# Kernel tuning notes

Hardware: AMD Instinct MI355X
Metric: run time of the kernel (lower is better)

Reference implementation:

```python
import jax, jax.numpy as jnp
import numpy as np

B, Q, S, T, H = 8, 64, 64, 64, 768
NH, HD = 12, 64  # head_num, head_dim


def setup_inputs() -> dict:
    key = jax.random.key(0)
    k1, k2, k3, k4, k5, k6, k7 = jax.random.split(key, 7)
    ini_q = jax.random.normal(k1, (B, Q, H), dtype=jnp.float32)
    ini_k = jax.random.normal(k2, (B, S, T, H), dtype=jnp.float32)
    mask = jax.random.randint(k3, (B, S, T), 0, 2).astype(jnp.float32)  # 1 = masked
    # learned params (Linear weights stored as [in, out] for x @ W)
    sc = 1.0 / np.sqrt(H)
    Wq = jax.random.normal(k4, (H, H), dtype=jnp.float32) * sc
    Wkv = jax.random.normal(k5, (H, H), dtype=jnp.float32) * sc
    Wo = jax.random.normal(k6, (H, H), dtype=jnp.float32) * sc
    bo = jax.random.normal(k7, (H,), dtype=jnp.float32) * 0.02
    return {"ini_q": ini_q, "ini_k": ini_k, "mask": mask,
            "Wq": Wq, "Wkv": Wkv, "Wo": Wo, "bo": bo}


def reference(ini_q, ini_k, mask, Wq, Wkv, Wo, bo):
    batch, q_num, _ = ini_q.shape
    _, s_num, t_num, _ = ini_k.shape
    scale = 1.0 / np.sqrt(HD)
    q = (ini_q @ Wq).reshape(batch, q_num, NH, HD)
    kv = (ini_k @ Wkv).reshape(batch, s_num, t_num, NH, HD)  # k == v
    # [b, h, q, s, t]
    scores = jnp.einsum('bqhd,bsthd->bhqst', q, kv) * scale
    scores = scores + mask[:, None, None, :, :] * -10000.0
    alpha = jax.nn.softmax(scores, axis=4)  # dropout is identity in eval
    res = jnp.einsum('bhqst,bsthd->bqshd', alpha, kv).reshape(batch, q_num, s_num, NH * HD)
    return res @ Wo + bo
```

## Files before the change

kernel.cpp:

```cpp
#include <hip/hip_runtime.h>
#include <stdint.h>


typedef __bf16 bf16_t;
typedef __attribute__((ext_vector_type(8))) __bf16 bf16x8;
typedef __attribute__((ext_vector_type(4))) __bf16 bf16x4;
typedef __attribute__((ext_vector_type(4))) float f32x4;

#define HDIM 768

__device__ __forceinline__ void gload16(const bf16_t* g, bf16_t* l) {
  __builtin_amdgcn_global_load_lds(
      (const __attribute__((address_space(1))) void*)g,
      (__attribute__((address_space(3))) void*)l, 16, 0, 0);
}

__global__ __launch_bounds__(256) void splitT_kernel(const float* __restrict__ w,
                                                     bf16_t* __restrict__ hT,
                                                     bf16_t* __restrict__ lT) {
  int idx = blockIdx.x * 256 + threadIdx.x;
  int k = idx / HDIM, n = idx % HDIM;
  float v = w[idx];
  bf16_t hb = (bf16_t)v;
  hT[n * HDIM + k] = hb;
  lT[n * HDIM + k] = (bf16_t)(v - (float)hb);
}

template <int EPI, bool AF32>
__global__ __launch_bounds__(256) void gemm_kernel(
    const float* __restrict__ Agf,
    const bf16_t* __restrict__ Agh, const bf16_t* __restrict__ Agl,
    const bf16_t* __restrict__ Bgh, const bf16_t* __restrict__ Bgl,
    bf16_t* __restrict__ Ch, bf16_t* __restrict__ Cl,
    bf16_t* __restrict__ CTh, bf16_t* __restrict__ CTl,
    float* __restrict__ Cf, const float* __restrict__ bias) {
  __shared__ bf16_t sAh[128 * 32], sAl[128 * 32], sBh[128 * 32], sBl[128 * 32];
  const int nwg = gridDim.x;
  const int cpx = nwg >> 3;
  const int g = blockIdx.x;
  const int wg = (g & 7) * cpx + (g >> 3);
  const int bn = wg % 6, bm = wg / 6;
  const int tid = threadIdx.x, lane = tid & 63, w = tid >> 6;
  const int wr = (w >> 1) * 64, wc = (w & 1) * 64;
  const int l15 = lane & 15, l4 = lane >> 4;
  f32x4 acc[4][4] = {};

  for (int kt = 0; kt < 24; ++kt) {
    const int k0 = kt * 32;
    __syncthreads();
    if constexpr (AF32) {
#pragma unroll
      for (int j = 0; j < 4; ++j) {
        const int c = tid + j * 256;
        const int row = c >> 3, cg = c & 7;
        const float4 v4 =
            *(const float4*)&Agf[(size_t)(bm * 128 + row) * HDIM + k0 + cg * 4];
        const float vv[4] = {v4.x, v4.y, v4.z, v4.w};
        bf16x4 hv, lv;
#pragma unroll
        for (int e = 0; e < 4; ++e) {
          bf16_t hb = (bf16_t)vv[e];
          hv[e] = hb;
          lv[e] = (bf16_t)(vv[e] - (float)hb);
        }
        *(bf16x4*)&sAh[row * 32 + cg * 4] = hv;
        *(bf16x4*)&sAl[row * 32 + cg * 4] = lv;
      }
    } else {
#pragma unroll
      for (int j = 0; j < 2; ++j) {
        const int c0 = j * 256 + w * 64;
        const int c = c0 + lane;
        const int row = c >> 2, cg = c & 3;
        const size_t ga = (size_t)(bm * 128 + row) * HDIM + k0 + cg * 8;
        gload16(&Agh[ga], &sAh[c0 * 8]);
        gload16(&Agl[ga], &sAl[c0 * 8]);
      }
    }
#pragma unroll
    for (int j = 0; j < 2; ++j) {
      const int c0 = j * 256 + w * 64;
      const int c = c0 + lane;
      const int row = c >> 2, cg = c & 3;
      const size_t gb = (size_t)(bn * 128 + row) * HDIM + k0 + cg * 8;
      gload16(&Bgh[gb], &sBh[c0 * 8]);
      gload16(&Bgl[gb], &sBl[c0 * 8]);
    }
    __syncthreads();
    bf16x8 a_h[4], a_l[4], b_h[4], b_l[4];
#pragma unroll
    for (int m = 0; m < 4; ++m) {
      const int ra = (wr + m * 16 + l15) * 32 + l4 * 8;
      a_h[m] = *(const bf16x8*)&sAh[ra];
      a_l[m] = *(const bf16x8*)&sAl[ra];
      const int rb = (wc + m * 16 + l15) * 32 + l4 * 8;
      b_h[m] = *(const bf16x8*)&sBh[rb];
      b_l[m] = *(const bf16x8*)&sBl[rb];
    }
#pragma unroll
    for (int m = 0; m < 4; ++m)
#pragma unroll
      for (int n = 0; n < 4; ++n) {
        acc[m][n] = __builtin_amdgcn_mfma_f32_16x16x32_bf16(a_h[m], b_h[n], acc[m][n], 0, 0, 0);
        acc[m][n] = __builtin_amdgcn_mfma_f32_16x16x32_bf16(a_h[m], b_l[n], acc[m][n], 0, 0, 0);
        acc[m][n] = __builtin_amdgcn_mfma_f32_16x16x32_bf16(a_l[m], b_h[n], acc[m][n], 0, 0, 0);
      }
  }
#pragma unroll
  for (int m = 0; m < 4; ++m)
#pragma unroll
    for (int n = 0; n < 4; ++n) {
      const int row0 = bm * 128 + wr + m * 16 + l4 * 4;
      const int col = bn * 128 + wc + n * 16 + l15;
      if constexpr (EPI == 1) {
        const float bv = bias[col];
#pragma unroll
        for (int j = 0; j < 4; ++j)
          Cf[(size_t)(row0 + j) * HDIM + col] = acc[m][n][j] + bv;
      } else if constexpr (EPI == 0) {
#pragma unroll
        for (int j = 0; j < 4; ++j) {
          const float v = acc[m][n][j];
          const bf16_t hb = (bf16_t)v;
          Ch[(size_t)(row0 + j) * HDIM + col] = hb;
          Cl[(size_t)(row0 + j) * HDIM + col] = (bf16_t)(v - (float)hb);
        }
      } else {
        bf16x4 hv, lv;
#pragma unroll
        for (int j = 0; j < 4; ++j) {
          const float v = acc[m][n][j];
          const bf16_t hb = (bf16_t)v;
          hv[j] = hb;
          lv[j] = (bf16_t)(v - (float)hb);
        }
        const int b = row0 >> 12, s = (row0 >> 6) & 63, t0 = row0 & 63;
        const int hh = col >> 6, d = col & 63;
        const size_t tb =
            ((size_t)((b * 64 + s) * 12 + hh)) * 4096 + d * 64 + t0;
        *(bf16x4*)&CTh[tb] = hv;
        *(bf16x4*)&CTl[tb] = lv;
      }
    }
}

__global__ __launch_bounds__(256) void attn_kernel(
    const bf16_t* __restrict__ qh, const bf16_t* __restrict__ ql,
    const bf16_t* __restrict__ kvTh, const bf16_t* __restrict__ kvTl,
    const float* __restrict__ mask,
    bf16_t* __restrict__ resh, bf16_t* __restrict__ resl) {
  const int s = blockIdx.x, hh = blockIdx.y, b = blockIdx.z;
  const int tid = threadIdx.x, lane = tid & 63, w = tid >> 6;
  const int l15 = lane & 15, l4 = lane >> 4;
  const int LDT = 72, LDP = 68;
  __shared__ __align__(16) char smemA[64 * 72 * 2 * 2];
  __shared__ __align__(16) bf16_t Ph[64 * 72], Pl[64 * 72];
  __shared__ float mk[64];
  bf16_t* Kh = (bf16_t*)smemA;
  bf16_t* Kl = Kh + 64 * 72;
  float* OldsF = (float*)smemA;

  if (tid < 64) mk[tid] = mask[((size_t)b * 64 + s) * 64 + tid] * -10000.0f;

  const size_t tb0 = ((size_t)((b * 64 + s) * 12 + hh)) * 4096;
#pragma unroll
  for (int j = 0; j < 2; ++j) {
    const int cg = j * 4 + w;
    const bf16x8 vh = *(const bf16x8*)&kvTh[tb0 + (size_t)lane * 64 + cg * 8];
    const bf16x8 vl = *(const bf16x8*)&kvTl[tb0 + (size_t)lane * 64 + cg * 8];
#pragma unroll
    for (int e = 0; e < 8; ++e) {
      Kh[(cg * 8 + e) * LDT + lane] = vh[e];
      Kl[(cg * 8 + e) * LDT + lane] = vl[e];
    }
  }

  const size_t qbase = ((size_t)(b * 64 + w * 16 + l15)) * HDIM + hh * 64;
  bf16x8 qh8[2], ql8[2];
#pragma unroll
  for (int ks = 0; ks < 2; ++ks) {
    qh8[ks] = *(const bf16x8*)&qh[qbase + ks * 32 + l4 * 8];
    ql8[ks] = *(const bf16x8*)&ql[qbase + ks * 32 + l4 * 8];
  }
  __syncthreads();

  f32x4 St[4] = {};
#pragma unroll
  for (int ks = 0; ks < 2; ++ks) {
#pragma unroll
    for (int mf = 0; mf < 4; ++mf) {
      const int ra = (mf * 16 + l15) * LDT + ks * 32 + l4 * 8;
      const bf16x8 kh8 = *(const bf16x8*)&Kh[ra];
      const bf16x8 kl8 = *(const bf16x8*)&Kl[ra];
      St[mf] = __builtin_amdgcn_mfma_f32_16x16x32_bf16(kh8, qh8[ks], St[mf], 0, 0, 0);
      St[mf] = __builtin_amdgcn_mfma_f32_16x16x32_bf16(kh8, ql8[ks], St[mf], 0, 0, 0);
      St[mf] = __builtin_amdgcn_mfma_f32_16x16x32_bf16(kl8, qh8[ks], St[mf], 0, 0, 0);
    }
  }

  float p[16];
  float mx = -1e30f;
#pragma unroll
  for (int mf = 0; mf < 4; ++mf)
#pragma unroll
    for (int j = 0; j < 4; ++j) {
      const float v = St[mf][j] * 0.125f + mk[mf * 16 + l4 * 4 + j];
      p[mf * 4 + j] = v;
      mx = fmaxf(mx, v);
    }
  mx = fmaxf(mx, __shfl_xor(mx, 16));
  mx = fmaxf(mx, __shfl_xor(mx, 32));
  float sum = 0.f;
#pragma unroll
  for (int i = 0; i < 16; ++i) {
    const float e = __expf(p[i] - mx);
    p[i] = e;
    sum += e;
  }
  sum += __shfl_xor(sum, 16);
  sum += __shfl_xor(sum, 32);
  const float inv = 1.0f / sum;

  const int q = w * 16 + l15;
#pragma unroll
  for (int mf = 0; mf < 4; ++mf) {
    bf16x4 hv, lv;
#pragma unroll
    for (int j = 0; j < 4; ++j) {
      const float v = p[mf * 4 + j] * inv;
      const bf16_t hb = (bf16_t)v;
      hv[j] = hb;
      lv[j] = (bf16_t)(v - (float)hb);
    }
    *(bf16x4*)&Ph[q * LDT + mf * 16 + l4 * 4] = hv;
    *(bf16x4*)&Pl[q * LDT + mf * 16 + l4 * 4] = lv;
  }
  __syncthreads();

  f32x4 Ot[4] = {};
  const size_t ab = tb0 + (size_t)(w * 16 + l15) * 64;
#pragma unroll
  for (int ks = 0; ks < 2; ++ks) {
    const bf16x8 ah = *(const bf16x8*)&kvTh[ab + ks * 32 + l4 * 8];
    const bf16x8 al = *(const bf16x8*)&kvTl[ab + ks * 32 + l4 * 8];
#pragma unroll
    for (int nf = 0; nf < 4; ++nf) {
      const int rb = (nf * 16 + l15) * LDT + ks * 32 + l4 * 8;
      const bf16x8 ph8 = *(const bf16x8*)&Ph[rb];
      const bf16x8 pl8 = *(const bf16x8*)&Pl[rb];
      Ot[nf] = __builtin_amdgcn_mfma_f32_16x16x32_bf16(ah, ph8, Ot[nf], 0, 0, 0);
      Ot[nf] = __builtin_amdgcn_mfma_f32_16x16x32_bf16(ah, pl8, Ot[nf], 0, 0, 0);
      Ot[nf] = __builtin_amdgcn_mfma_f32_16x16x32_bf16(al, ph8, Ot[nf], 0, 0, 0);
    }
  }
#pragma unroll
  for (int nf = 0; nf < 4; ++nf)
    *(f32x4*)&OldsF[(nf * 16 + l15) * LDP + w * 16 + l4 * 4] = Ot[nf];
  __syncthreads();

  const int qq = tid >> 2, ch = tid & 3;
  float vv[16];
#pragma unroll
  for (int k = 0; k < 4; ++k) {
    const f32x4 t4 = *(const f32x4*)&OldsF[qq * LDP + ch * 16 + k * 4];
    vv[k * 4 + 0] = t4[0]; vv[k * 4 + 1] = t4[1];
    vv[k * 4 + 2] = t4[2]; vv[k * 4 + 3] = t4[3];
  }
  bf16x8 h8[2], l8[2];
#pragma unroll
  for (int k = 0; k < 16; ++k) {
    const float v = vv[k];
    const bf16_t hb = (bf16_t)v;
    h8[k >> 3][k & 7] = hb;
    l8[k >> 3][k & 7] = (bf16_t)(v - (float)hb);
  }
  const size_t rb = ((size_t)((b * 64 + qq) * 64 + s)) * HDIM + hh * 64 + ch * 16;
  *(bf16x8*)&resh[rb] = h8[0];
  *(bf16x8*)&resh[rb + 8] = h8[1];
  *(bf16x8*)&resl[rb] = l8[0];
  *(bf16x8*)&resl[rb + 8] = l8[1];
}

extern "C" void kernel_launch(void* const* d_in, const int* in_sizes, int n_in,
                              void* d_out, int out_size, void* d_ws, size_t ws_size,
                              hipStream_t stream) {
  const float* ini_q = (const float*)d_in[0];
  const float* ini_k = (const float*)d_in[1];
  const float* mask = (const float*)d_in[2];
  const float* Wq = (const float*)d_in[3];
  const float* Wkv = (const float*)d_in[4];
  const float* Wo = (const float*)d_in[5];
  const float* bo = (const float*)d_in[6];
  float* out = (float*)d_out;

  const size_t SQ = 512ull * HDIM;
  const size_t SK = 32768ull * HDIM;
  const size_t SW = 768ull * HDIM;

  char* p = (char*)d_ws;
  auto carve = [&](size_t bytes) {
    char* r = p;
    p += (bytes + 255) & ~(size_t)255;
    return r;
  };
  bf16_t* wq_h = (bf16_t*)carve(SW * 2);
  bf16_t* wq_l = (bf16_t*)carve(SW * 2);
  bf16_t* wkv_h = (bf16_t*)carve(SW * 2);
  bf16_t* wkv_l = (bf16_t*)carve(SW * 2);
  bf16_t* wo_h = (bf16_t*)carve(SW * 2);
  bf16_t* wo_l = (bf16_t*)carve(SW * 2);
  bf16_t* q_h = (bf16_t*)carve(SQ * 2);
  bf16_t* q_l = (bf16_t*)carve(SQ * 2);
  bf16_t* kvT_h = (bf16_t*)carve(SK * 2);
  bf16_t* kvT_l = (bf16_t*)carve(SK * 2);
  bf16_t* res_h = (bf16_t*)carve(SK * 2);
  bf16_t* res_l = (bf16_t*)carve(SK * 2);
  if ((size_t)(p - (char*)d_ws) > ws_size) return;

  splitT_kernel<<<dim3(SW / 256), 256, 0, stream>>>(Wq, wq_h, wq_l);
  splitT_kernel<<<dim3(SW / 256), 256, 0, stream>>>(Wkv, wkv_h, wkv_l);
  splitT_kernel<<<dim3(SW / 256), 256, 0, stream>>>(Wo, wo_h, wo_l);

  gemm_kernel<0, true><<<dim3(24), 256, 0, stream>>>(
      ini_q, nullptr, nullptr, wq_h, wq_l, q_h, q_l, nullptr, nullptr,
      nullptr, nullptr);
  gemm_kernel<2, true><<<dim3(1536), 256, 0, stream>>>(
      ini_k, nullptr, nullptr, wkv_h, wkv_l, nullptr, nullptr, kvT_h, kvT_l,
      nullptr, nullptr);
  attn_kernel<<<dim3(64, 12, 8), 256, 0, stream>>>(q_h, q_l, kvT_h, kvT_l,
                                                   mask, res_h, res_l);
  gemm_kernel<1, false><<<dim3(1536), 256, 0, stream>>>(
      nullptr, res_h, res_l, wo_h, wo_l, nullptr, nullptr, nullptr, nullptr,
      out, bo);
}
```

Baseline: 541.9 us.

## Restructure attention to loop over s with double-buffered K and dual KV layouts

The KV projection GEMM now writes both a transposed and a natural-layout copy of the split bf16 KV. The attention kernel processes 8 s-slices per block, double-buffering the natural-layout K tile into XOR-swizzled LDS via async global-to-LDS loads, and reads V directly from global in transposed layout. It also writes results directly instead of transposing through LDS. GEMM LDS tiles get XOR swizzling or padding to reduce bank conflicts. The cost is extra global writes for the second KV copy and scattered 2-byte result stores.

```diff
diff --git a/kernel.cpp b/kernel.cpp
--- a/kernel.cpp
+++ b/kernel.cpp
@@ -33,8 +33,11 @@
     const bf16_t* __restrict__ Bgh, const bf16_t* __restrict__ Bgl,
     bf16_t* __restrict__ Ch, bf16_t* __restrict__ Cl,
     bf16_t* __restrict__ CTh, bf16_t* __restrict__ CTl,
+    bf16_t* __restrict__ CNh, bf16_t* __restrict__ CNl,
     float* __restrict__ Cf, const float* __restrict__ bias) {
-  __shared__ bf16_t sAh[128 * 32], sAl[128 * 32], sBh[128 * 32], sBl[128 * 32];
+  const int LDA = AF32 ? 40 : 32;
+  __shared__ bf16_t sAh[128 * 40], sAl[128 * 40];
+  __shared__ bf16_t sBh[128 * 32], sBl[128 * 32];
   const int nwg = gridDim.x;
   const int cpx = nwg >> 3;
   const int g = blockIdx.x;
@@ -63,16 +66,17 @@
           hv[e] = hb;
           lv[e] = (bf16_t)(vv[e] - (float)hb);
         }
-        *(bf16x4*)&sAh[row * 32 + cg * 4] = hv;
-        *(bf16x4*)&sAl[row * 32 + cg * 4] = lv;
+        *(bf16x4*)&sAh[row * 40 + cg * 4] = hv;
+        *(bf16x4*)&sAl[row * 40 + cg * 4] = lv;
       }
     } else {
 #pragma unroll
       for (int j = 0; j < 2; ++j) {
         const int c0 = j * 256 + w * 64;
         const int c = c0 + lane;
-        const int row = c >> 2, cg = c & 3;
-        const size_t ga = (size_t)(bm * 128 + row) * HDIM + k0 + cg * 8;
+        const int row = c >> 2, slot = c & 3;
+        const size_t ga = (size_t)(bm * 128 + row) * HDIM + k0 +
+                          ((slot ^ ((row >> 1) & 3)) * 8);
         gload16(&Agh[ga], &sAh[c0 * 8]);
         gload16(&Agl[ga], &sAl[c0 * 8]);
       }
@@ -81,8 +85,9 @@
     for (int j = 0; j < 2; ++j) {
       const int c0 = j * 256 + w * 64;
       const int c = c0 + lane;
-      const int row = c >> 2, cg = c & 3;
-      const size_t gb = (size_t)(bn * 128 + row) * HDIM + k0 + cg * 8;
+      const int row = c >> 2, slot = c & 3;
+      const size_t gb = (size_t)(bn * 128 + row) * HDIM + k0 +
+                        ((slot ^ ((row >> 1) & 3)) * 8);
       gload16(&Bgh[gb], &sBh[c0 * 8]);
       gload16(&Bgl[gb], &sBl[c0 * 8]);
     }
@@ -90,10 +95,13 @@
     bf16x8 a_h[4], a_l[4], b_h[4], b_l[4];
 #pragma unroll
     for (int m = 0; m < 4; ++m) {
-      const int ra = (wr + m * 16 + l15) * 32 + l4 * 8;
+      const int rowa = wr + m * 16 + l15;
+      const int ra = AF32 ? rowa * 40 + l4 * 8
+                          : rowa * 32 + ((l4 ^ ((rowa >> 1) & 3)) * 8);
       a_h[m] = *(const bf16x8*)&sAh[ra];
       a_l[m] = *(const bf16x8*)&sAl[ra];
-      const int rb = (wc + m * 16 + l15) * 32 + l4 * 8;
+      const int rowb = wc + m * 16 + l15;
+      const int rb = rowb * 32 + ((l4 ^ ((rowb >> 1) & 3)) * 8);
       b_h[m] = *(const bf16x8*)&sBh[rb];
       b_l[m] = *(const bf16x8*)&sBl[rb];
     }
@@ -136,149 +144,159 @@
         }
         const int b = row0 >> 12, s = (row0 >> 6) & 63, t0 = row0 & 63;
         const int hh = col >> 6, d = col & 63;
-        const size_t tb =
-            ((size_t)((b * 64 + s) * 12 + hh)) * 4096 + d * 64 + t0;
-        *(bf16x4*)&CTh[tb] = hv;
-        *(bf16x4*)&CTl[tb] = lv;
-      }
-    }
-}
-
-__global__ __launch_bounds__(256) void attn_kernel(
+        const size_t base = ((size_t)((b * 64 + s) * 12 + hh)) * 4096;
+        *(bf16x4*)&CTh[base + d * 64 + t0] = hv;
+        *(bf16x4*)&CTl[base + d * 64 + t0] = lv;
+#pragma unroll
+        for (int j = 0; j < 4; ++j) {
+          CNh[base + (t0 + j) * 64 + d] = hv[j];
+          CNl[base + (t0 + j) * 64 + d] = lv[j];
+        }
+      }
+    }
+}
+
+__device__ __forceinline__ void stage_k(const bf16_t* __restrict__ gh,
+                                        const bf16_t* __restrict__ gl,
+                                        bf16_t* lh, bf16_t* ll,
+                                        int w, int lane) {
+#pragma unroll
+  for (int j = 0; j < 2; ++j) {
+    const int c0 = j * 256 + w * 64;
+    const int c = c0 + lane;
+    const int t = c >> 3, sl = c & 7;
+    const int srcd = (sl ^ (t & 7)) * 8;
+    gload16(&gh[t * 64 + srcd], &lh[c0 * 8]);
+    gload16(&gl[t * 64 + srcd], &ll[c0 * 8]);
+  }
+}
+
+__global__ __launch_bounds__(256, 3) void attn_kernel(
     const bf16_t* __restrict__ qh, const bf16_t* __restrict__ ql,
+    const bf16_t* __restrict__ kvNh, const bf16_t* __restrict__ kvNl,
     const bf16_t* __restrict__ kvTh, const bf16_t* __restrict__ kvTl,
     const float* __restrict__ mask,
     bf16_t* __restrict__ resh, bf16_t* __restrict__ resl) {
-  const int s = blockIdx.x, hh = blockIdx.y, b = blockIdx.z;
+  const int sq = blockIdx.x, hh = blockIdx.y, b = blockIdx.z;
+  const int s0 = sq * 8;
   const int tid = threadIdx.x, lane = tid & 63, w = tid >> 6;
   const int l15 = lane & 15, l4 = lane >> 4;
-  const int LDT = 72, LDP = 68;
-  __shared__ __align__(16) char smemA[64 * 72 * 2 * 2];
-  __shared__ __align__(16) bf16_t Ph[64 * 72], Pl[64 * 72];
-  __shared__ float mk[64];
-  bf16_t* Kh = (bf16_t*)smemA;
-  bf16_t* Kl = Kh + 64 * 72;
-  float* OldsF = (float*)smemA;
-
-  if (tid < 64) mk[tid] = mask[((size_t)b * 64 + s) * 64 + tid] * -10000.0f;
-
-  const size_t tb0 = ((size_t)((b * 64 + s) * 12 + hh)) * 4096;
-#pragma unroll
-  for (int j = 0; j < 2; ++j) {
-    const int cg = j * 4 + w;
-    const bf16x8 vh = *(const bf16x8*)&kvTh[tb0 + (size_t)lane * 64 + cg * 8];
-    const bf16x8 vl = *(const bf16x8*)&kvTl[tb0 + (size_t)lane * 64 + cg * 8];
-#pragma unroll
-    for (int e = 0; e < 8; ++e) {
-      Kh[(cg * 8 + e) * LDT + lane] = vh[e];
-      Kl[(cg * 8 + e) * LDT + lane] = vl[e];
-    }
+  __shared__ bf16_t Ksm[2][2][64 * 64];
+  __shared__ bf16_t Ph[64 * 72], Pl[64 * 72];
+  __shared__ float mk[8 * 64];
+
+  {
+    const int i2 = tid * 2;
+    const float2 mv = *(const float2*)
+        &mask[((size_t)(b * 64 + s0 + (i2 >> 6))) * 64 + (i2 & 63)];
+    mk[i2] = mv.x * -10000.0f;
+    mk[i2 + 1] = mv.y * -10000.0f;
   }
 
   const size_t qbase = ((size_t)(b * 64 + w * 16 + l15)) * HDIM + hh * 64;
-  bf16x8 qh8[2], ql8[2];
+  bf16x8 qf_h[2], qf_l[2];
 #pragma unroll
   for (int ks = 0; ks < 2; ++ks) {
-    qh8[ks] = *(const bf16x8*)&qh[qbase + ks * 32 + l4 * 8];
-    ql8[ks] = *(const bf16x8*)&ql[qbase + ks * 32 + l4 * 8];
-  }
+    qf_h[ks] = *(const bf16x8*)&qh[qbase + ks * 32 + l4 * 8];
+    qf_l[ks] = *(const bf16x8*)&ql[qbase + ks * 32 + l4 * 8];
+  }
+
+  const size_t hb0 = ((size_t)((b * 64 + s0) * 12 + hh)) * 4096;
+  const size_t SSTR = 12 * 4096;
+
+  stage_k(&kvNh[hb0], &kvNl[hb0], &Ksm[0][0][0], &Ksm[0][1][0], w, lane);
   __syncthreads();
 
-  f32x4 St[4] = {};
-#pragma unroll
-  for (int ks = 0; ks < 2; ++ks) {
+  const int q = w * 16 + l15;
+  for (int si = 0; si < 8; ++si) {
+    const int cur = si & 1;
+    const int sn = (si < 7) ? si + 1 : 7;
+    stage_k(&kvNh[hb0 + sn * SSTR], &kvNl[hb0 + sn * SSTR],
+            &Ksm[cur ^ 1][0][0], &Ksm[cur ^ 1][1][0], w, lane);
+
+    f32x4 St[4] = {};
+#pragma unroll
+    for (int ks = 0; ks < 2; ++ks) {
+#pragma unroll
+      for (int mf = 0; mf < 4; ++mf) {
+        const int t = mf * 16 + l15;
+        const int off = t * 64 + (((ks * 4 + l4) ^ (t & 7)) * 8);
+        const bf16x8 kh8 = *(const bf16x8*)&Ksm[cur][0][off];
+        const bf16x8 kl8 = *(const bf16x8*)&Ksm[cur][1][off];
+        St[mf] = __builtin_amdgcn_mfma_f32_16x16x32_bf16(kh8, qf_h[ks], St[mf], 0, 0, 0);
+        St[mf] = __builtin_amdgcn_mfma_f32_16x16x32_bf16(kh8, qf_l[ks], St[mf], 0, 0, 0);
+        St[mf] = __builtin_amdgcn_mfma_f32_16x16x32_bf16(kl8, qf_h[ks], St[mf], 0, 0, 0);
+      }
+    }
+
+    float p[16];
+    float mx = -1e30f;
+#pragma unroll
+    for (int mf = 0; mf < 4; ++mf)
+#pragma unroll
+      for (int j = 0; j < 4; ++j) {
+        const float v = St[mf][j] * 0.125f + mk[si * 64 + mf * 16 + l4 * 4 + j];
+        p[mf * 4 + j] = v;
+        mx = fmaxf(mx, v);
+      }
+    mx = fmaxf(mx, __shfl_xor(mx, 16));
+    mx = fmaxf(mx, __shfl_xor(mx, 32));
+    float sum = 0.f;
+#pragma unroll
+    for (int i = 0; i < 16; ++i) {
+      const float e = __expf(p[i] - mx);
+      p[i] = e;
+      sum += e;
+    }
+    sum += __shfl_xor(sum, 16);
+    sum += __shfl_xor(sum, 32);
+    const float inv = 1.0f / sum;
+
 #pragma unroll
     for (int mf = 0; mf < 4; ++mf) {
-      const int ra = (mf * 16 + l15) * LDT + ks * 32 + l4 * 8;
-      const bf16x8 kh8 = *(const bf16x8*)&Kh[ra];
-      const bf16x8 kl8 = *(const bf16x8*)&Kl[ra];
-      St[mf] = __builtin_amdgcn_mfma_f32_16x16x32_bf16(kh8, qh8[ks], St[mf], 0, 0, 0);
-      St[mf] = __builtin_amdgcn_mfma_f32_16x16x32_bf16(kh8, ql8[ks], St[mf], 0, 0, 0);
-      St[mf] = __builtin_amdgcn_mfma_f32_16x16x32_bf16(kl8, qh8[ks], St[mf], 0, 0, 0);
-    }
-  }
-
-  float p[16];
-  float mx = -1e30f;
-#pragma unroll
-  for (int mf = 0; mf < 4; ++mf)
-#pragma unroll
-    for (int j = 0; j < 4; ++j) {
-      const float v = St[mf][j] * 0.125f + mk[mf * 16 + l4 * 4 + j];
-      p[mf * 4 + j] = v;
-      mx = fmaxf(mx, v);
-    }
-  mx = fmaxf(mx, __shfl_xor(mx, 16));
-  mx = fmaxf(mx, __shfl_xor(mx, 32));
-  float sum = 0.f;
-#pragma unroll
-  for (int i = 0; i < 16; ++i) {
-    const float e = __expf(p[i] - mx);
-    p[i] = e;
-    sum += e;
-  }
-  sum += __shfl_xor(sum, 16);
-  sum += __shfl_xor(sum, 32);
-  const float inv = 1.0f / sum;
-
-  const int q = w * 16 + l15;
-#pragma unroll
-  for (int mf = 0; mf < 4; ++mf) {
-    bf16x4 hv, lv;
-#pragma unroll
-    for (int j = 0; j < 4; ++j) {
-      const float v = p[mf * 4 + j] * inv;
-      const bf16_t hb = (bf16_t)v;
-      hv[j] = hb;
-      lv[j] = (bf16_t)(v - (float)hb);
-    }
-    *(bf16x4*)&Ph[q * LDT + mf * 16 + l4 * 4] = hv;
-    *(bf16x4*)&Pl[q * LDT + mf * 16 + l4 * 4] = lv;
-  }
-  __syncthreads();
-
-  f32x4 Ot[4] = {};
-  const size_t ab = tb0 + (size_t)(w * 16 + l15) * 64;
-#pragma unroll
-  for (int ks = 0; ks < 2; ++ks) {
-    const bf16x8 ah = *(const bf16x8*)&kvTh[ab + ks * 32 + l4 * 8];
-    const bf16x8 al = *(const bf16x8*)&kvTl[ab + ks * 32 + l4 * 8];
-#pragma unroll
-    for (int nf = 0; nf < 4; ++nf) {
-      const int rb = (nf * 16 + l15) * LDT + ks * 32 + l4 * 8;
-      const bf16x8 ph8 = *(const bf16x8*)&Ph[rb];
-      const bf16x8 pl8 = *(const bf16x8*)&Pl[rb];
-      Ot[nf] = __builtin_amdgcn_mfma_f32_16x16x32_bf16(ah, ph8, Ot[nf], 0, 0, 0);
-      Ot[nf] = __builtin_amdgcn_mfma_f32_16x16x32_bf16(ah, pl8, Ot[nf], 0, 0, 0);
-      Ot[nf] = __builtin_amdgcn_mfma_f32_16x16x32_bf16(al, ph8, Ot[nf], 0, 0, 0);
-    }
-  }
-#pragma unroll
-  for (int nf = 0; nf < 4; ++nf)
-    *(f32x4*)&OldsF[(nf * 16 + l15) * LDP + w * 16 + l4 * 4] = Ot[nf];
-  __syncthreads();
-
-  const int qq = tid >> 2, ch = tid & 3;
-  float vv[16];
-#pragma unroll
-  for (int k = 0; k < 4; ++k) {
-    const f32x4 t4 = *(const f32x4*)&OldsF[qq * LDP + ch * 16 + k * 4];
-    vv[k * 4 + 0] = t4[0]; vv[k * 4 + 1] = t4[1];
-    vv[k * 4 + 2] = t4[2]; vv[k * 4 + 3] = t4[3];
-  }
-  bf16x8 h8[2], l8[2];
-#pragma unroll
-  for (int k = 0; k < 16; ++k) {
-    const float v = vv[k];
-    const bf16_t hb = (bf16_t)v;
-    h8[k >> 3][k & 7] = hb;
-    l8[k >> 3][k & 7] = (bf16_t)(v - (float)hb);
-  }
-  const size_t rb = ((size_t)((b * 64 + qq) * 64 + s)) * HDIM + hh * 64 + ch * 16;
-  *(bf16x8*)&resh[rb] = h8[0];
-  *(bf16x8*)&resh[rb + 8] = h8[1];
-  *(bf16x8*)&resl[rb] = l8[0];
-  *(bf16x8*)&resl[rb + 8] = l8[1];
+      bf16x4 hv, lv;
+#pragma unroll
+      for (int j = 0; j < 4; ++j) {
+        const float v = p[mf * 4 + j] * inv;
+        const bf16_t hb = (bf16_t)v;
+        hv[j] = hb;
+        lv[j] = (bf16_t)(v - (float)hb);
+      }
+      *(bf16x4*)&Ph[q * 72 + mf * 16 + l4 * 4] = hv;
+      *(bf16x4*)&Pl[q * 72 + mf * 16 + l4 * 4] = lv;
+    }
+
+    f32x4 O[4] = {};
+    const size_t tb = hb0 + si * SSTR;
+#pragma unroll
+    for (int ks = 0; ks < 2; ++ks) {
+      const bf16x8 pa = *(const bf16x8*)&Ph[q * 72 + ks * 32 + l4 * 8];
+      const bf16x8 pb = *(const bf16x8*)&Pl[q * 72 + ks * 32 + l4 * 8];
+#pragma unroll
+      for (int nf = 0; nf < 4; ++nf) {
+        const size_t bb = tb + (size_t)(nf * 16 + l15) * 64 + ks * 32 + l4 * 8;
+        const bf16x8 vh = *(const bf16x8*)&kvTh[bb];
+        const bf16x8 vl = *(const bf16x8*)&kvTl[bb];
+        O[nf] = __builtin_amdgcn_mfma_f32_16x16x32_bf16(pa, vh, O[nf], 0, 0, 0);
+        O[nf] = __builtin_amdgcn_mfma_f32_16x16x32_bf16(pa, vl, O[nf], 0, 0, 0);
+        O[nf] = __builtin_amdgcn_mfma_f32_16x16x32_bf16(pb, vh, O[nf], 0, 0, 0);
+      }
+    }
+    __syncthreads();
+
+#pragma unroll
+    for (int nf = 0; nf < 4; ++nf)
+#pragma unroll
+      for (int j = 0; j < 4; ++j) {
+        const int qo = w * 16 + l4 * 4 + j;
+        const size_t idx =
+            ((size_t)((b * 64 + qo) * 64 + s0 + si)) * HDIM + hh * 64 + nf * 16 + l15;
+        const float v = O[nf][j];
+        const bf16_t hb = (bf16_t)v;
+        resh[idx] = hb;
+        resl[idx] = (bf16_t)(v - (float)hb);
+      }
+  }
 }
 
 extern "C" void kernel_launch(void* const* d_in, const int* in_sizes, int n_in,
@@ -313,6 +331,8 @@
   bf16_t* q_l = (bf16_t*)carve(SQ * 2);
   bf16_t* kvT_h = (bf16_t*)carve(SK * 2);
   bf16_t* kvT_l = (bf16_t*)carve(SK * 2);
+  bf16_t* kvN_h = (bf16_t*)carve(SK * 2);
+  bf16_t* kvN_l = (bf16_t*)carve(SK * 2);
   bf16_t* res_h = (bf16_t*)carve(SK * 2);
   bf16_t* res_l = (bf16_t*)carve(SK * 2);
   if ((size_t)(p - (char*)d_ws) > ws_size) return;
@@ -323,13 +343,13 @@
 
   gemm_kernel<0, true><<<dim3(24), 256, 0, stream>>>(
       ini_q, nullptr, nullptr, wq_h, wq_l, q_h, q_l, nullptr, nullptr,
-      nullptr, nullptr);
-  gemm_kernel<2, true><<<dim3(1536), 256, 0, stream>>>(
+      nullptr, nullptr, nullptr, nullptr);
+  gemm_kernel<3, true><<<dim3(1536), 256, 0, stream>>>(
       ini_k, nullptr, nullptr, wkv_h, wkv_l, nullptr, nullptr, kvT_h, kvT_l,
-      nullptr, nullptr);
-  attn_kernel<<<dim3(64, 12, 8), 256, 0, stream>>>(q_h, q_l, kvT_h, kvT_l,
-                                                   mask, res_h, res_l);
+      kvN_h, kvN_l, nullptr, nullptr);
+  attn_kernel<<<dim3(8, 12, 8), 256, 0, stream>>>(
+      q_h, q_l, kvN_h, kvN_l, kvT_h, kvT_l, mask, res_h, res_l);
   gemm_kernel<1, false><<<dim3(1536), 256, 0, stream>>>(
       nullptr, res_h, res_l, wo_h, wo_l, nullptr, nullptr, nullptr, nullptr,
-      out, bo);
-}
+      nullptr, nullptr, out, bo);
+}
```

Measured after the change: 639.9 us. +18.1%, slower.
